# Optimization experiments

Hardware: AMD Instinct MI355X
Metric: run time of the kernel (lower is better)

Reference implementation:

```python
import jax, jax.numpy as jnp
import numpy as np

B, N, C, K3, KNN = 4, 4096, 128, 3, 16
SCALE = 1.0 / np.sqrt(C)  # attention uses sqrt(embed_dim)
EPS = 1e-5


def _knn_idx(x, k):
    # squared euclidean distances (monotone in cdist), topk smallest
    x2 = jnp.sum(x * x, axis=-1)                       # [B,N]
    d2 = x2[:, :, None] + x2[:, None, :] - 2.0 * jnp.einsum('bnd,bmd->bnm', x, x)
    _, idx = jax.lax.top_k(-d2, k)                     # [B,N,k]
    return idx


def _gather(x, idx):
    # knn_gather: x [B,N,D], idx [B,N,k] -> [B,N,k,D]
    return jax.vmap(lambda xb, ib: xb[ib])(x, idx)


def _attn(q_in, kv_in, Wq, Wk, Wv):
    # q_in [B,N,D], kv_in [B,N,k,D]; torch Linear: x @ W.T
    Q = q_in @ Wq.T
    Kt = kv_in @ Wk.T
    V = kv_in @ Wv.T
    scores = jnp.einsum('bnkd,bnd->bnk', Kt, Q) * SCALE
    a = jax.nn.softmax(scores, axis=-1)
    return jnp.einsum('bnk,bnkd->bnd', a, V)


def _ln(x, g, b):
    mu = jnp.mean(x, axis=-1, keepdims=True)
    var = jnp.mean((x - mu) ** 2, axis=-1, keepdims=True)
    return (x - mu) * jax.lax.rsqrt(var + EPS) * g + b


def setup_inputs() -> dict:
    key = jax.random.key(0)
    ks = jax.random.split(key, 20)
    s = 0.05
    inp = {
        'src': jax.random.normal(ks[0], (B, N, K3), dtype=jnp.float32),
        'tgt': jax.random.normal(ks[1], (B, N, C), dtype=jnp.float32),
        'Wq0': jax.random.normal(ks[2], (C, C), dtype=jnp.float32) * s,
        'Wk0': jax.random.normal(ks[3], (C, C), dtype=jnp.float32) * s,
        'Wv0': jax.random.normal(ks[4], (C, C), dtype=jnp.float32) * s,
        'Wq1': jax.random.normal(ks[5], (C, C), dtype=jnp.float32) * s,
        'Wk1': jax.random.normal(ks[6], (C, C), dtype=jnp.float32) * s,
        'Wv1': jax.random.normal(ks[7], (C, C), dtype=jnp.float32) * s,
        'Wp0': jax.random.normal(ks[8], (C, K3), dtype=jnp.float32) * s,
        'bp0': jnp.zeros((C,), dtype=jnp.float32),
        'Wp1': jax.random.normal(ks[9], (C, C), dtype=jnp.float32) * s,
        'bp1': jnp.zeros((C,), dtype=jnp.float32),
        'Wl': jax.random.normal(ks[10], (C, C), dtype=jnp.float32) * s,
        'bl': jnp.zeros((C,), dtype=jnp.float32),
        'g0': jnp.ones((C,), dtype=jnp.float32),
        'b0': jnp.zeros((C,), dtype=jnp.float32),
        'g1': jnp.ones((C,), dtype=jnp.float32),
        'b1': jnp.zeros((C,), dtype=jnp.float32),
    }
    return inp


def reference(src, tgt, Wq0, Wk0, Wv0, Wq1, Wk1, Wv1, Wp0, bp0, Wp1, bp1, Wl, bl, g0, b0, g1, b1):
    k = min(KNN, src.shape[1])
    # stage 1: knn on coordinates
    idx = _knn_idx(src, k)
    gather_src = _gather(src, idx)                         # [B,N,k,3]
    residual_src = (src[:, :, None, :] - gather_src) @ Wp0.T + bp0
    gather_tgt = _gather(tgt, idx)                         # [B,N,k,C]
    out = _attn(tgt, residual_src + gather_tgt, Wq0, Wk0, Wv0)
    # stage 2: knn in feature space
    idx2 = _knn_idx(out, k)
    gather_out = _gather(out, idx2)
    residual_out = (out[:, :, None, :] - gather_out) @ Wp1.T + bp1
    out = _attn(out, residual_out + gather_out, Wq1, Wk1, Wv1)
    out_0 = tgt + out
    out_1 = _ln(out_0, g0, b0) @ Wl.T + bl
    out_2 = _ln(tgt + out_1, g1, b1)
    return jnp.transpose(out_2, (1, 0, 2))                 # [N,B,C]
```

## Files before the change

### kernel.cpp

```cpp
#include <hip/hip_runtime.h>
#include <math.h>

#define NB 4
#define NN 4096
#define NC 128
#define NROWS (NB*NN)
#define SCALE_F 0.08838834764831845f

using bf16x8 = __attribute__((ext_vector_type(8))) short;
using f32x4  = __attribute__((ext_vector_type(4))) float;

__device__ __forceinline__ float rl_f(float x, int l) {
    return __int_as_float(__builtin_amdgcn_readlane(__float_as_int(x), l));
}
__device__ __forceinline__ ushort f2bf(float x) {
    unsigned u = __float_as_uint(x);
    return (ushort)((u + 0x7FFF + ((u >> 16) & 1)) >> 16);
}
__device__ __forceinline__ float bf2f(ushort b) { return __uint_as_float(((unsigned)b) << 16); }

__device__ __forceinline__ unsigned long long mkkey(float d2, int idx) {
    unsigned u = __float_as_uint(d2);
    u ^= ((unsigned)((int)u >> 31)) | 0x80000000u;
    return ((unsigned long long)u << 32) | (unsigned)idx;
}

#define DECL16V \
    float v0=INFINITY,v1=INFINITY,v2=INFINITY,v3=INFINITY,v4=INFINITY,v5=INFINITY,v6=INFINITY,v7=INFINITY, \
          v8=INFINITY,v9=INFINITY,v10=INFINITY,v11=INFINITY,v12=INFINITY,v13=INFINITY,v14=INFINITY,v15=INFINITY;

#define INSERT16V(dv) do { float d_=(dv); \
    bool m0=d_<v0,m1=d_<v1,m2=d_<v2,m3=d_<v3,m4=d_<v4,m5=d_<v5,m6=d_<v6,m7=d_<v7, \
         m8=d_<v8,m9=d_<v9,m10=d_<v10,m11=d_<v11,m12=d_<v12,m13=d_<v13,m14=d_<v14,m15=d_<v15; \
    v15=m14?v14:(m15?d_:v15); v14=m13?v13:(m14?d_:v14); v13=m12?v12:(m13?d_:v13); v12=m11?v11:(m12?d_:v12); \
    v11=m10?v10:(m11?d_:v11); v10=m9?v9:(m10?d_:v10); v9 =m8?v8:(m9?d_:v9);  v8 =m7?v7:(m8?d_:v8); \
    v7 =m6?v6:(m7?d_:v7);   v6 =m5?v5:(m6?d_:v6);   v5 =m4?v4:(m5?d_:v5);  v4 =m3?v3:(m4?d_:v4); \
    v3 =m2?v2:(m3?d_:v3);   v2 =m1?v1:(m2?d_:v2);   v1 =m0?v0:(m1?d_:v1);  v0 =m0?d_:v0; } while(0)

#define POP16V(p) do { bool p_=(p); \
    v0=p_?v1:v0; v1=p_?v2:v1; v2=p_?v3:v2; v3=p_?v4:v3; v4=p_?v5:v4; v5=p_?v6:v5; v6=p_?v7:v6; v7=p_?v8:v7; \
    v8=p_?v9:v8; v9=p_?v10:v9; v10=p_?v11:v10; v11=p_?v12:v11; v12=p_?v13:v12; v13=p_?v14:v13; v14=p_?v15:v14; \
    v15=p_?INFINITY:v15; } while(0)

#define KMAX16 0xFFFFFFFFFFFFFFFFull
#define DECL16K \
    unsigned long long K0=KMAX16,K1=KMAX16,K2=KMAX16,K3=KMAX16,K4=KMAX16,K5=KMAX16,K6=KMAX16,K7=KMAX16, \
                       K8=KMAX16,K9=KMAX16,K10=KMAX16,K11=KMAX16,K12=KMAX16,K13=KMAX16,K14=KMAX16,K15=KMAX16;

#define INSERT16K(kv) do { unsigned long long k_=(kv); \
    bool m0=k_<K0,m1=k_<K1,m2=k_<K2,m3=k_<K3,m4=k_<K4,m5=k_<K5,m6=k_<K6,m7=k_<K7, \
         m8=k_<K8,m9=k_<K9,m10=k_<K10,m11=k_<K11,m12=k_<K12,m13=k_<K13,m14=k_<K14,m15=k_<K15; \
    K15=m14?K14:(m15?k_:K15); K14=m13?K13:(m14?k_:K14); K13=m12?K12:(m13?k_:K13); K12=m11?K11:(m12?k_:K12); \
    K11=m10?K10:(m11?k_:K11); K10=m9?K9:(m10?k_:K10);   K9 =m8?K8:(m9?k_:K9);    K8 =m7?K7:(m8?k_:K8); \
    K7 =m6?K6:(m7?k_:K7);     K6 =m5?K5:(m6?k_:K6);     K5 =m4?K4:(m5?k_:K5);    K4 =m3?K3:(m4?k_:K4); \
    K3 =m2?K2:(m3?k_:K3);     K2 =m1?K1:(m2?k_:K2);     K1 =m0?K0:(m1?k_:K1);    K0 =m0?k_:K0; } while(0)

#define POP16K(p) do { bool p_=(p); \
    K0=p_?K1:K0; K1=p_?K2:K1; K2=p_?K3:K2; K3=p_?K4:K3; K4=p_?K5:K4; K5=p_?K6:K5; K6=p_?K7:K6; K7=p_?K8:K7; \
    K8=p_?K9:K8; K9=p_?K10:K9; K10=p_?K11:K10; K11=p_?K12:K11; K12=p_?K13:K12; K13=p_?K14:K13; K14=p_?K15:K14; \
    K15=p_?KMAX16:K15; } while(0)

__global__ void combo_small(const float* __restrict__ Wk0, const float* __restrict__ Wv0,
                            const float* __restrict__ Wp0, const float* __restrict__ bp0,
                            float* __restrict__ WKP0, float* __restrict__ BK0,
                            float* __restrict__ WVP0, float* __restrict__ BV0)
{
    int task = blockIdx.x * 512 + threadIdx.x;
    if (task >= 1024) return;
    int mat = task >> 9; int rem = task & 511;
    int c = rem >> 2, t = rem & 3;
    const float* W = mat ? Wv0 : Wk0;
    float s = 0.f;
    if (t < 3) {
        for (int d = 0; d < 128; ++d) s = fmaf(W[c*128+d], Wp0[d*3+t], s);
        (mat ? WVP0 : WKP0)[c*3+t] = s;
    } else {
        for (int d = 0; d < 128; ++d) s = fmaf(W[c*128+d], bp0[d], s);
        (mat ? BV0 : BK0)[c] = s;
    }
}

__global__ void combo_big(const float* __restrict__ Wk1, const float* __restrict__ Wv1,
                          const float* __restrict__ Wp1, const float* __restrict__ bp1,
                          float* __restrict__ WKD, float* __restrict__ MV1,
                          float* __restrict__ WVD, float* __restrict__ BV1)
{
    int task = blockIdx.x * 256 + threadIdx.x;
    if (task >= 32896) return;
    if (task < 32768) {
        int mat = task >> 14; int rem = task & 16383;
        int c = rem >> 7, tcol = rem & 127;
        const float* W = mat ? Wv1 : Wk1;
        float s = 0.f;
        for (int d = 0; d < 128; ++d) s = fmaf(W[c*128+d], Wp1[d*128+tcol], s);
        if (mat) { MV1[rem] = s; WVD[rem] = Wv1[rem] - s; }
        else     { WKD[rem] = Wk1[rem] - s; }
    } else {
        int c = task - 32768;
        float s = 0.f;
        for (int d = 0; d < 128; ++d) s = fmaf(Wv1[c*128+d], bp1[d], s);
        BV1[c] = s;
    }
}

__global__ void srcproj(const float* __restrict__ src, const float* __restrict__ WKP0,
                        const float* __restrict__ WVP0,
                        float* __restrict__ srcKp, float* __restrict__ srcVp)
{
    int gid = blockIdx.x * 256 + threadIdx.x;
    int i = gid >> 7, c = gid & 127;
    float s0 = src[i*3+0], s1 = src[i*3+1], s2 = src[i*3+2];
    srcKp[gid] = fmaf(s0, WKP0[c*3+0], fmaf(s1, WKP0[c*3+1], s2*WKP0[c*3+2]));
    srcVp[gid] = fmaf(s0, WVP0[c*3+0], fmaf(s1, WVP0[c*3+1], s2*WVP0[c*3+2]));
}

__global__ __launch_bounds__(256) void knn1_kernel(const float* __restrict__ src,
                                                   int* __restrict__ idxout)
{
    int lane = threadIdx.x & 63, wave = threadIdx.x >> 6;
    int b7 = blockIdx.x & 7, sub = blockIdx.x >> 3;
    int batch = b7 >> 1;
    int rib = (sub*2 + (b7 & 1))*4 + wave;
    int row = batch*NN + rib;
    const float* sb = src + batch*NN*3;
    float xi0 = sb[rib*3], xi1 = sb[rib*3+1], xi2 = sb[rib*3+2];

    DECL16V
    for (int it = 0; it < 64; ++it) {
        int j = it*64 + lane;
        float dx = xi0 - sb[j*3], dy = xi1 - sb[j*3+1], dz = xi2 - sb[j*3+2];
        float d2 = fmaf(dx, dx, fmaf(dy, dy, dz*dz));
        if (d2 < v15) INSERT16V(d2);
    }
    float T = INFINITY;
    for (int t = 0; t < 16; ++t) {
        float g = v0;
#pragma unroll
        for (int off = 1; off < 64; off <<= 1) g = fminf(g, __shfl_xor(g, off, 64));
        unsigned long long b = __ballot(v0 == g);
        int f = __ffsll((long long)b) - 1;
        POP16V(lane == f);
        T = g;
    }
    unsigned long long below_mask = (lane == 63) ? 0x7fffffffffffffffull : ((1ull << lane) - 1ull);
    int base = 0;
    for (int it = 0; it < 64; ++it) {
        int j = it*64 + lane;
        float dx = xi0 - sb[j*3], dy = xi1 - sb[j*3+1], dz = xi2 - sb[j*3+2];
        float d2 = fmaf(dx, dx, fmaf(dy, dy, dz*dz));
        unsigned long long blt = __ballot(d2 < T);
        if (d2 < T) idxout[row*16 + base + __popcll(blt & below_mask)] = j;
        base += __popcll(blt);
    }
    for (int it = 0; it < 64 && base < 16; ++it) {
        int j = it*64 + lane;
        float dx = xi0 - sb[j*3], dy = xi1 - sb[j*3+1], dz = xi2 - sb[j*3+2];
        float d2 = fmaf(dx, dx, fmaf(dy, dy, dz*dz));
        unsigned long long beq = __ballot(d2 == T);
        int bel = __popcll(beq & below_mask);
        if (d2 == T && base + bel < 16) idxout[row*16 + base + bel] = j;
        base += __popcll(beq);
    }
}

__device__ __forceinline__ void matmul128_body(const float* __restrict__ X,
                                               const float* __restrict__ W,
                                               const float* __restrict__ S,
                                               float* __restrict__ Y)
{
    __shared__ float WL[128*128];
    int tid = threadIdx.x;
    for (int f = tid; f < 16384; f += 256) {
        int c = f >> 7, d = f & 127;
        WL[d*128 + (c ^ (d & 14))] = W[f];
    }
    __syncthreads();
    int lane = tid & 63, wave = tid >> 6;
#pragma unroll
    for (int it = 0; it < 2; ++it) {
        int row0 = blockIdx.x*32 + it*16 + wave*4;
        float2 xp[4];
#pragma unroll
        for (int r = 0; r < 4; ++r) {
            xp[r] = *(const float2*)&X[(row0+r)*128 + 2*lane];
        }
        float2 acc[4];
#pragma unroll
        for (int r = 0; r < 4; ++r) { acc[r].x = 0.f; acc[r].y = 0.f; }
#pragma unroll 8
        for (int dh = 0; dh < 64; ++dh) {
            int cidx = (2*lane) ^ ((2*dh) & 14);
            float2 wa = *(const float2*)&WL[(2*dh)*128 + cidx];
            float2 wb = *(const float2*)&WL[(2*dh+1)*128 + cidx];
#pragma unroll
            for (int r = 0; r < 4; ++r) {
                float xa = rl_f(xp[r].x, dh);
                float xb = rl_f(xp[r].y, dh);
                acc[r].x = fmaf(xa, wa.x, acc[r].x);
                acc[r].y = fmaf(xa, wa.y, acc[r].y);
                acc[r].x = fmaf(xb, wb.x, acc[r].x);
                acc[r].y = fmaf(xb, wb.y, acc[r].y);
            }
        }
#pragma unroll
        for (int r = 0; r < 4; ++r) {
            float2 o = acc[r];
            if (S != nullptr) {
                float2 s2 = *(const float2*)&S[(row0+r)*128 + 2*lane];
                o.x -= s2.x; o.y -= s2.y;
            }
            *(float2*)&Y[(row0+r)*128 + 2*lane] = o;
        }
    }
}

__global__ __launch_bounds__(256) void matmul128x3s(
    const float* __restrict__ X,
    const float* __restrict__ W0, const float* __restrict__ W1, const float* __restrict__ W2,
    const float* __restrict__ S1, const float* __restrict__ S2,
    float* __restrict__ Y0, float* __restrict__ Y1, float* __restrict__ Y2)
{
    if (blockIdx.y == 0)      matmul128_body(X, W0, nullptr, Y0);
    else if (blockIdx.y == 1) matmul128_body(X, W1, S1, Y1);
    else                      matmul128_body(X, W2, S2, Y2);
}

__global__ __launch_bounds__(256) void matmul128x4(
    const float* __restrict__ X,
    const float* __restrict__ W0, const float* __restrict__ W1,
    const float* __restrict__ W2, const float* __restrict__ W3,
    float* __restrict__ Y0, float* __restrict__ Y1,
    float* __restrict__ Y2, float* __restrict__ Y3)
{
    const float* W; float* Y;
    switch (blockIdx.y) {
        case 0: W = W0; Y = Y0; break;
        case 1: W = W1; Y = Y1; break;
        case 2: W = W2; Y = Y2; break;
        default: W = W3; Y = Y3; break;
    }
    matmul128_body(X, W, nullptr, Y);
}

__global__ __launch_bounds__(512) void attn_kernel(
    const float* __restrict__ Q,  const float* __restrict__ GK, const float* __restrict__ GV,
    const float* __restrict__ BASE, const float* __restrict__ bv,
    const int* __restrict__ idx, float* __restrict__ outp, float* __restrict__ x2out,
    ushort* __restrict__ xh, ushort* __restrict__ xl)
{
    int tid = threadIdx.x;
    int lane = tid & 63, wave = tid >> 6;
    int xcd = blockIdx.x & 7, sub = blockIdx.x >> 3;
    int batch = xcd >> 1;
    int band = sub*2 + (xcd & 1);
    int rgrp = lane >> 4;
    int dimg = lane & 15;
    int rib = band*32 + wave*4 + rgrp;
    int row = batch*NN + rib;
    int d0 = dimg*8;
    int gbase = lane & 48;
    const float* GKb = GK + (size_t)batch*NN*NC;
    const float* GVb = GV + (size_t)batch*NN*NC;

    float4 q0 = *(const float4*)&Q[(size_t)row*NC + d0];
    float4 q1 = *(const float4*)&Q[(size_t)row*NC + d0 + 4];
    int jv = idx[row*16 + dimg];

    float sc[16];
#pragma unroll
    for (int k = 0; k < 16; ++k) {
        int j = __shfl(jv, gbase + k, 64);
        const float* gk = &GKb[(size_t)j*NC + d0];
        float4 g0 = *(const float4*)gk;
        float4 g1 = *(const float4*)(gk + 4);
        float p = fmaf(q0.x, g0.x, fmaf(q0.y, g0.y, fmaf(q0.z, g0.z, fmaf(q0.w, g0.w,
                  fmaf(q1.x, g1.x, fmaf(q1.y, g1.y, fmaf(q1.z, g1.z, q1.w*g1.w)))))));
#pragma unroll
        for (int off = 1; off < 16; off <<= 1) p += __shfl_xor(p, off, 64);
        sc[k] = p * SCALE_F;
    }
    float m = sc[0];
#pragma unroll
    for (int k = 1; k < 16; ++k) m = fmaxf(m, sc[k]);
    float wsum = 0.f, w[16];
#pragma unroll
    for (int k = 0; k < 16; ++k) { w[k] = expf(sc[k] - m); wsum += w[k]; }
    float inv = 1.f / wsum;

    float4 a0 = {0.f,0.f,0.f,0.f}, a1 = {0.f,0.f,0.f,0.f};
#pragma unroll
    for (int k = 0; k < 16; ++k) {
        int j = __shfl(jv, gbase + k, 64);
        const float* gv = &GVb[(size_t)j*NC + d0];
        float4 v0 = *(const float4*)gv;
        float4 v1 = *(const float4*)(gv + 4);
        float a = w[k] * inv;
        a0.x = fmaf(a, v0.x, a0.x); a0.y = fmaf(a, v0.y, a0.y);
        a0.z = fmaf(a, v0.z, a0.z); a0.w = fmaf(a, v0.w, a0.w);
        a1.x = fmaf(a, v1.x, a1.x); a1.y = fmaf(a, v1.y, a1.y);
        a1.z = fmaf(a, v1.z, a1.z); a1.w = fmaf(a, v1.w, a1.w);
    }
    float4 b0 = *(const float4*)&BASE[(size_t)row*NC + d0];
    float4 b1 = *(const float4*)&BASE[(size_t)row*NC + d0 + 4];
    float4 c0 = *(const float4*)&bv[d0];
    float4 c1 = *(const float4*)&bv[d0 + 4];
    a0.x += b0.x + c0.x; a0.y += b0.y + c0.y; a0.z += b0.z + c0.z; a0.w += b0.w + c0.w;
    a1.x += b1.x + c1.x; a1.y += b1.y + c1.y; a1.z += b1.z + c1.z; a1.w += b1.w + c1.w;
    *(float4*)&outp[(size_t)row*NC + d0]     = a0;
    *(float4*)&outp[(size_t)row*NC + d0 + 4] = a1;

    if (x2out != nullptr) {
        float x2 = fmaf(a0.x, a0.x, fmaf(a0.y, a0.y, fmaf(a0.z, a0.z, fmaf(a0.w, a0.w,
                   fmaf(a1.x, a1.x, fmaf(a1.y, a1.y, fmaf(a1.z, a1.z, a1.w*a1.w)))))));
#pragma unroll
        for (int off = 1; off < 16; off <<= 1) x2 += __shfl_xor(x2, off, 64);
        if (dimg == 0) x2out[row] = x2;
    }
    if (xh != nullptr) {
        ushort h0 = f2bf(a0.x), h1 = f2bf(a0.y), h2 = f2bf(a0.z), h3 = f2bf(a0.w);
        ushort h4 = f2bf(a1.x), h5 = f2bf(a1.y), h6 = f2bf(a1.z), h7 = f2bf(a1.w);
        uint4 ph;
        ph.x = (unsigned)h0 | ((unsigned)h1 << 16);
        ph.y = (unsigned)h2 | ((unsigned)h3 << 16);
        ph.z = (unsigned)h4 | ((unsigned)h5 << 16);
        ph.w = (unsigned)h6 | ((unsigned)h7 << 16);
        *(uint4*)&xh[(size_t)row*NC + d0] = ph;
        ushort l0 = f2bf(a0.x - bf2f(h0)), l1 = f2bf(a0.y - bf2f(h1));
        ushort l2 = f2bf(a0.z - bf2f(h2)), l3 = f2bf(a0.w - bf2f(h3));
        ushort l4 = f2bf(a1.x - bf2f(h4)), l5 = f2bf(a1.y - bf2f(h5));
        ushort l6 = f2bf(a1.z - bf2f(h6)), l7 = f2bf(a1.w - bf2f(h7));
        uint4 pl;
        pl.x = (unsigned)l0 | ((unsigned)l1 << 16);
        pl.y = (unsigned)l2 | ((unsigned)l3 << 16);
        pl.z = (unsigned)l4 | ((unsigned)l5 << 16);
        pl.w = (unsigned)l6 | ((unsigned)l7 << 16);
        *(uint4*)&xl[(size_t)row*NC + d0] = pl;
    }
}

#define SCAN_STEP(CP, X2S, REFRESH) do { \
    float4 dd = *(const float4*)&DT[dtrd]; \
    float4 xx = *(const float4*)&(X2S)[slotl*4]; \
    int cb = 0; \
    { float d2 = fmaf(-2.f, dd.x, xx.x); bool p = d2 <= Trow; \
      unsigned long long bal = __ballot(p); unsigned grp = (unsigned)(bal >> grpsh) & 0xFFFFu; \
      if (p) BUF[srow][cb + __popc(grp & lowm)] = mkkey(d2, (CP) + slotl*4 + 0); \
      cb += __popc(grp); } \
    { float d2 = fmaf(-2.f, dd.y, xx.y); bool p = d2 <= Trow; \
      unsigned long long bal = __ballot(p); unsigned grp = (unsigned)(bal >> grpsh) & 0xFFFFu; \
      if (p) BUF[srow][cb + __popc(grp & lowm)] = mkkey(d2, (CP) + slotl*4 + 1); \
      cb += __popc(grp); } \
    { float d2 = fmaf(-2.f, dd.z, xx.z); bool p = d2 <= Trow; \
      unsigned long long bal = __ballot(p); unsigned grp = (unsigned)(bal >> grpsh) & 0xFFFFu; \
      if (p) BUF[srow][cb + __popc(grp & lowm)] = mkkey(d2, (CP) + slotl*4 + 2); \
      cb += __popc(grp); } \
    { float d2 = fmaf(-2.f, dd.w, xx.w); bool p = d2 <= Trow; \
      unsigned long long bal = __ballot(p); unsigned grp = (unsigned)(bal >> grpsh) & 0xFFFFu; \
      if (p) BUF[srow][cb + __popc(grp & lowm)] = mkkey(d2, (CP) + slotl*4 + 3); \
      cb += __popc(grp); } \
    _Pragma("unroll") \
    for (int r = 0; r < 4; ++r) { \
        int ii = r*16 + slotl; \
        if (ii < cb) { \
            unsigned long long k = BUF[srow][ii]; \
            if (k < K15) INSERT16K(k); \
        } \
    } \
    if (REFRESH) { \
        unsigned long long tk = K15; \
        _Pragma("unroll") \
        for (int off = 1; off < 16; off <<= 1) { \
            unsigned long long o = __shfl_xor(tk, off, 64); \
            tk = (o < tk) ? o : tk; \
        } \
        unsigned uu = (unsigned)(tk >> 32); \
        uu = (uu > 0xFF800000u) ? 0xFF800000u : uu; \
        uu = (uu & 0x80000000u) ? (uu ^ 0x80000000u) : ~uu; \
        Trow = __uint_as_float(uu); \
    } \
} while (0)

__global__ __launch_bounds__(512, 2) void knn2_kernel(const ushort* __restrict__ XHg,
                                                      const ushort* __restrict__ XLg,
                                                      const float* __restrict__ x2g,
                                                      int* __restrict__ idxout)
{
    __shared__ __align__(16) ushort XCH[64*128];
    __shared__ __align__(16) ushort XCL[64*128];
    __shared__ __align__(16) float  DT[32*64];
    __shared__ unsigned long long   BUF[32][65];
    __shared__ __align__(16) float  X2T[2][64];
    int tid = threadIdx.x;
    int lane = tid & 63, wave = tid >> 6;
    int xcd = blockIdx.x & 7, sub = blockIdx.x >> 3;
    int batch = xcd >> 1;
    int band = sub*2 + (xcd & 1);
    const ushort* XHb = XHg + (size_t)batch*NN*NC;
    const ushort* XLb = XLg + (size_t)batch*NN*NC;
    const float*  x2b = x2g + (size_t)batch*NN;
    int r0 = band*32;

    int rowblk = wave & 1, colblk = wave >> 1;
    int dbase = (lane >> 4) * 8;
    int gr = r0 + rowblk*16 + (lane & 15);
    bf16x8 AH[4], AL[4];
#pragma unroll
    for (int ks = 0; ks < 4; ++ks) {
        AH[ks] = *(const bf16x8*)&XHb[(size_t)gr*NC + ks*32 + dbase];
        AL[ks] = *(const bf16x8*)&XLb[(size_t)gr*NC + ks*32 + dbase];
    }
    int cB = colblk*16 + (lane & 15);
    int colw = colblk*16 + (lane & 15);

    int srow = tid >> 4, slotl = tid & 15;
    int grpsh = lane & 48;
    unsigned lowm = (1u << slotl) - 1u;
    int dtrd = srow*64 + ((slotl*4 + 4*srow) & 63);
    float Trow = INFINITY;
    DECL16K

    for (int t = 0; t < 64; ++t) {
        int c0 = t*64;
        __syncthreads();
#pragma unroll
        for (int i = 0; i < 2; ++i) {
            int qq = tid + 512*i;
            int c = qq >> 4, d8 = qq & 15;
            int widx = c*128 + ((d8*8) ^ ((c & 7) << 3));
            *(uint4*)&XCH[widx] = *(const uint4*)&XHb[(size_t)(c0 + c)*NC + d8*8];
            *(uint4*)&XCL[widx] = *(const uint4*)&XLb[(size_t)(c0 + c)*NC + d8*8];
        }
        if (tid < 64) X2T[t & 1][tid] = x2b[c0 + tid];
        if (t > 0) {
            const float* x2s = X2T[(t - 1) & 1];
            SCAN_STEP(c0 - 64, x2s, 1);
        }
        __syncthreads();
        f32x4 acc = {0.f, 0.f, 0.f, 0.f};
#pragma unroll
        for (int ks = 0; ks < 4; ++ks) {
            int bidx = cB*128 + ((ks*32 + dbase) ^ ((cB & 7) << 3));
            bf16x8 bh = *(const bf16x8*)&XCH[bidx];
            bf16x8 bl = *(const bf16x8*)&XCL[bidx];
            acc = __builtin_amdgcn_mfma_f32_16x16x32_bf16(AH[ks], bh, acc, 0, 0, 0);
            acc = __builtin_amdgcn_mfma_f32_16x16x32_bf16(AL[ks], bh, acc, 0, 0, 0);
            acc = __builtin_amdgcn_mfma_f32_16x16x32_bf16(AH[ks], bl, acc, 0, 0, 0);
        }
#pragma unroll
        for (int r2 = 0; r2 < 4; ++r2) {
            int rA = rowblk*16 + (lane >> 4)*4 + r2;
            DT[rA*64 + (((colw & ~3) + 4*rA) & 63) + (colw & 3)] = acc[r2];
        }
    }
    __syncthreads();
    {
        const float* x2s = X2T[1];
        SCAN_STEP(63*64, x2s, 0);
    }
    int grow = batch*NN + r0 + srow;
    for (int tt = 0; tt < 16; ++tt) {
        unsigned long long g = K0;
#pragma unroll
        for (int off = 1; off < 16; off <<= 1) {
            unsigned long long o = __shfl_xor(g, off, 64);
            g = (o < g) ? o : g;
        }
        bool win = (K0 == g);
        if (win) idxout[grow*16 + tt] = (int)(unsigned)(g & 0xFFFFFFFFull);
        POP16K(win);
    }
}

__global__ __launch_bounds__(256) void final_kernel(
    const float* __restrict__ tgt, const float* __restrict__ att,
    const float* __restrict__ Wl, const float* __restrict__ bl,
    const float* __restrict__ g0, const float* __restrict__ b0,
    const float* __restrict__ g1, const float* __restrict__ b1,
    float* __restrict__ outp)
{
    __shared__ float WL[128*128];
    int tid = threadIdx.x;
    for (int f = tid; f < 16384; f += 256) {
        int c = f >> 7, d = f & 127;
        WL[d*128 + (c ^ (d & 14))] = Wl[f];
    }
    __syncthreads();
    int lane = tid & 63, wave = tid >> 6;
    float2 gg0 = *(const float2*)&g0[2*lane];
    float2 bb0 = *(const float2*)&b0[2*lane];
    float2 gg1 = *(const float2*)&g1[2*lane];
    float2 bb1 = *(const float2*)&b1[2*lane];
    float2 bl2 = *(const float2*)&bl[2*lane];
    for (int it = 0; it < 4; ++it) {
        int row0 = blockIdx.x*64 + it*16 + wave*4;
        float2 tg[4];
        float lnx[4], lny[4];
#pragma unroll
        for (int r = 0; r < 4; ++r) {
            int row = row0 + r;
            tg[r] = *(const float2*)&tgt[row*128 + 2*lane];
            float2 at = *(const float2*)&att[row*128 + 2*lane];
            float ox = tg[r].x + at.x, oy = tg[r].y + at.y;
            float s = ox + oy;
#pragma unroll
            for (int off = 1; off < 64; off <<= 1) s += __shfl_xor(s, off, 64);
            float mu = s * (1.f/128.f);
            float dx = ox - mu, dy = oy - mu;
            float vv = fmaf(dx, dx, dy*dy);
#pragma unroll
            for (int off = 1; off < 64; off <<= 1) vv += __shfl_xor(vv, off, 64);
            float rstd = rsqrtf(vv * (1.f/128.f) + 1e-5f);
            lnx[r] = dx * rstd * gg0.x + bb0.x;
            lny[r] = dy * rstd * gg0.y + bb0.y;
        }
        float2 acc[4];
#pragma unroll
        for (int r = 0; r < 4; ++r) { acc[r].x = 0.f; acc[r].y = 0.f; }
#pragma unroll 8
        for (int dh = 0; dh < 64; ++dh) {
            int cidx = (2*lane) ^ ((2*dh) & 14);
            float2 wa = *(const float2*)&WL[(2*dh)*128 + cidx];
            float2 wb = *(const float2*)&WL[(2*dh+1)*128 + cidx];
#pragma unroll
            for (int r = 0; r < 4; ++r) {
                float xa = rl_f(lnx[r], dh);
                float xb = rl_f(lny[r], dh);
                acc[r].x = fmaf(xa, wa.x, acc[r].x);
                acc[r].y = fmaf(xa, wa.y, acc[r].y);
                acc[r].x = fmaf(xb, wb.x, acc[r].x);
                acc[r].y = fmaf(xb, wb.y, acc[r].y);
            }
        }
#pragma unroll
        for (int r = 0; r < 4; ++r) {
            int row = row0 + r;
            float zx = tg[r].x + acc[r].x + bl2.x;
            float zy = tg[r].y + acc[r].y + bl2.y;
            float s = zx + zy;
#pragma unroll
            for (int off = 1; off < 64; off <<= 1) s += __shfl_xor(s, off, 64);
            float mu = s * (1.f/128.f);
            float dx = zx - mu, dy = zy - mu;
            float vv = fmaf(dx, dx, dy*dy);
#pragma unroll
            for (int off = 1; off < 64; off <<= 1) vv += __shfl_xor(vv, off, 64);
            float rstd = rsqrtf(vv * (1.f/128.f) + 1e-5f);
            float2 res;
            res.x = dx * rstd * gg1.x + bb1.x;
            res.y = dy * rstd * gg1.y + bb1.y;
            int b = row >> 12, n = row & 4095;
            *(float2*)&outp[((size_t)n*NB + b)*128 + 2*lane] = res;
        }
    }
}

extern "C" void kernel_launch(void* const* d_in, const int* in_sizes, int n_in,
                              void* d_out, int out_size, void* d_ws, size_t ws_size,
                              hipStream_t stream)
{
    (void)in_sizes; (void)n_in; (void)out_size; (void)ws_size;
    const float* src = (const float*)d_in[0];
    const float* tgt = (const float*)d_in[1];
    const float* Wq0 = (const float*)d_in[2];
    const float* Wk0 = (const float*)d_in[3];
    const float* Wv0 = (const float*)d_in[4];
    const float* Wq1 = (const float*)d_in[5];
    const float* Wk1 = (const float*)d_in[6];
    const float* Wv1 = (const float*)d_in[7];
    const float* Wp0 = (const float*)d_in[8];
    const float* bp0 = (const float*)d_in[9];
    const float* Wp1 = (const float*)d_in[10];
    const float* bp1 = (const float*)d_in[11];
    const float* Wl  = (const float*)d_in[12];
    const float* bl  = (const float*)d_in[13];
    const float* g0  = (const float*)d_in[14];
    const float* b0  = (const float*)d_in[15];
    const float* g1  = (const float*)d_in[16];
    const float* b1  = (const float*)d_in[17];
    float* out = (float*)d_out;

    float* A0   = (float*)d_ws;
    float* A1   = A0 + 2097152;
    float* A2   = A1 + 2097152;
    float* A3   = A2 + 2097152;
    float* A4   = A3 + 2097152;
    float* OUT1 = A4 + 2097152;
    int*   IDX1 = (int*)(OUT1 + 2097152);
    int*   IDX2 = IDX1 + NROWS*16;
    float* X2G  = (float*)(IDX2 + NROWS*16);
    float* WKP0 = X2G + NROWS;
    float* BK0  = WKP0 + 384;
    float* WVP0 = BK0 + 128;
    float* BV0  = WVP0 + 384;
    float* WKD  = BV0 + 128;
    float* MV1  = WKD + 16384;
    float* WVD  = MV1 + 16384;
    float* BV1  = WVD + 16384;
    ushort* XH  = (ushort*)(BV1 + 128);
    ushort* XL  = XH + (size_t)NROWS*NC;

    combo_small<<<dim3(2), dim3(512), 0, stream>>>(Wk0, Wv0, Wp0, bp0, WKP0, BK0, WVP0, BV0);
    combo_big<<<dim3(129), dim3(256), 0, stream>>>(Wk1, Wv1, Wp1, bp1, WKD, MV1, WVD, BV1);
    srcproj<<<dim3(8192), dim3(256), 0, stream>>>(src, WKP0, WVP0, A3, A4);
    knn1_kernel<<<dim3(4096), dim3(256), 0, stream>>>(src, IDX1);
    matmul128x3s<<<dim3(512, 3), dim3(256), 0, stream>>>(tgt, Wq0, Wk0, Wv0, A3, A4, A0, A1, A2);
    attn_kernel<<<dim3(512), dim3(512), 0, stream>>>(A0, A1, A2, A4, BV0, IDX1, OUT1, X2G, XH, XL);
    knn2_kernel<<<dim3(512), dim3(512), 0, stream>>>(XH, XL, X2G, IDX2);
    matmul128x4<<<dim3(512, 4), dim3(256), 0, stream>>>(OUT1, Wq1, WKD, WVD, MV1, A0, A1, A2, A3);
    attn_kernel<<<dim3(512), dim3(512), 0, stream>>>(A0, A1, A2, A3, BV1, IDX2, OUT1, nullptr, nullptr, nullptr);
    final_kernel<<<dim3(256), dim3(256), 0, stream>>>(tgt, OUT1, Wl, bl, g0, b0, g1, b1, out);
}
```

Measured before the change: 499.9 us.

## Replace FP32 scalar projection GEMMs with split-bf16 MFMA GEMM

Replaces the scalar FP32 readlane-based 128x128 projection matmuls with an MFMA kernel that splits inputs and weights into bf16 high and low parts and sums three products, approximating FP32 accuracy. It adds kernels that pre-split the weights and the tgt input. The second-stage GEMM reuses the XH/XL split already emitted by the first attention kernel. This moves the projection work from FP32 vector ALUs to matrix cores, at the cost of extra conversion launches and a small precision loss from dropping the low-times-low term.

```diff
diff --git a/kernel.cpp b/kernel.cpp
--- a/kernel.cpp
+++ b/kernel.cpp
@@ -103,6 +103,46 @@
     }
 }
 
+__global__ void split7(const float* __restrict__ W0, const float* __restrict__ W1,
+                       const float* __restrict__ W2, const float* __restrict__ W3,
+                       const float* __restrict__ W4, const float* __restrict__ W5,
+                       const float* __restrict__ W6,
+                       ushort* __restrict__ WSH, ushort* __restrict__ WSL)
+{
+    int y = blockIdx.y;
+    const float* W;
+    switch (y) {
+        case 0: W = W0; break; case 1: W = W1; break; case 2: W = W2; break;
+        case 3: W = W3; break; case 4: W = W4; break; case 5: W = W5; break;
+        default: W = W6; break;
+    }
+    int i = blockIdx.x*256 + threadIdx.x;
+    float v = W[i];
+    ushort h = f2bf(v);
+    WSH[y*16384 + i] = h;
+    WSL[y*16384 + i] = f2bf(v - bf2f(h));
+}
+
+__global__ void splitx(const float* __restrict__ X, ushort* __restrict__ XH,
+                       ushort* __restrict__ XL)
+{
+    int i = (blockIdx.x*256 + threadIdx.x) * 8;
+    float4 a = *(const float4*)&X[i];
+    float4 b = *(const float4*)&X[i+4];
+    ushort h0=f2bf(a.x),h1=f2bf(a.y),h2=f2bf(a.z),h3=f2bf(a.w);
+    ushort h4=f2bf(b.x),h5=f2bf(b.y),h6=f2bf(b.z),h7=f2bf(b.w);
+    uint4 ph;
+    ph.x=(unsigned)h0|((unsigned)h1<<16); ph.y=(unsigned)h2|((unsigned)h3<<16);
+    ph.z=(unsigned)h4|((unsigned)h5<<16); ph.w=(unsigned)h6|((unsigned)h7<<16);
+    *(uint4*)&XH[i] = ph;
+    ushort l0=f2bf(a.x-bf2f(h0)),l1=f2bf(a.y-bf2f(h1)),l2=f2bf(a.z-bf2f(h2)),l3=f2bf(a.w-bf2f(h3));
+    ushort l4=f2bf(b.x-bf2f(h4)),l5=f2bf(b.y-bf2f(h5)),l6=f2bf(b.z-bf2f(h6)),l7=f2bf(b.w-bf2f(h7));
+    uint4 pl;
+    pl.x=(unsigned)l0|((unsigned)l1<<16); pl.y=(unsigned)l2|((unsigned)l3<<16);
+    pl.z=(unsigned)l4|((unsigned)l5<<16); pl.w=(unsigned)l6|((unsigned)l7<<16);
+    *(uint4*)&XL[i] = pl;
+}
+
 __global__ void srcproj(const float* __restrict__ src, const float* __restrict__ WKP0,
                         const float* __restrict__ WVP0,
                         float* __restrict__ srcKp, float* __restrict__ srcVp)
@@ -163,83 +203,59 @@
     }
 }
 
-__device__ __forceinline__ void matmul128_body(const float* __restrict__ X,
-                                               const float* __restrict__ W,
-                                               const float* __restrict__ S,
-                                               float* __restrict__ Y)
-{
-    __shared__ float WL[128*128];
-    int tid = threadIdx.x;
-    for (int f = tid; f < 16384; f += 256) {
-        int c = f >> 7, d = f & 127;
-        WL[d*128 + (c ^ (d & 14))] = W[f];
+__global__ __launch_bounds__(256, 2) void gemm128(
+    const ushort* __restrict__ XHg, const ushort* __restrict__ XLg,
+    const ushort* __restrict__ WHb, const ushort* __restrict__ WLb,
+    const float* __restrict__ S1, const float* __restrict__ S2,
+    float* __restrict__ Ybase)
+{
+    __shared__ __align__(16) ushort WHs[128*128];
+    __shared__ __align__(16) ushort WLs[128*128];
+    int tid = threadIdx.x, lane = tid & 63, wave = tid >> 6;
+    int y = blockIdx.y;
+    const ushort* WH = WHb + y*16384;
+    const ushort* WL = WLb + y*16384;
+    float* Y = Ybase + (size_t)y*2097152;
+    const float* S = (y == 1) ? S1 : ((y == 2) ? S2 : nullptr);
+#pragma unroll
+    for (int i = 0; i < 8; ++i) {
+        int q = tid + 256*i;
+        int c = q >> 4, d8 = q & 15;
+        int widx = c*128 + ((d8*8) ^ ((c & 7) << 3));
+        *(uint4*)&WHs[widx] = *(const uint4*)&WH[c*128 + d8*8];
+        *(uint4*)&WLs[widx] = *(const uint4*)&WL[c*128 + d8*8];
+    }
+    int r = blockIdx.x*64 + wave*16 + (lane & 15);
+    int dbase = (lane >> 4) * 8;
+    bf16x8 AH[4], AL[4];
+#pragma unroll
+    for (int ks = 0; ks < 4; ++ks) {
+        AH[ks] = *(const bf16x8*)&XHg[(size_t)r*128 + ks*32 + dbase];
+        AL[ks] = *(const bf16x8*)&XLg[(size_t)r*128 + ks*32 + dbase];
     }
     __syncthreads();
-    int lane = tid & 63, wave = tid >> 6;
-#pragma unroll
-    for (int it = 0; it < 2; ++it) {
-        int row0 = blockIdx.x*32 + it*16 + wave*4;
-        float2 xp[4];
-#pragma unroll
-        for (int r = 0; r < 4; ++r) {
-            xp[r] = *(const float2*)&X[(row0+r)*128 + 2*lane];
-        }
-        float2 acc[4];
-#pragma unroll
-        for (int r = 0; r < 4; ++r) { acc[r].x = 0.f; acc[r].y = 0.f; }
-#pragma unroll 8
-        for (int dh = 0; dh < 64; ++dh) {
-            int cidx = (2*lane) ^ ((2*dh) & 14);
-            float2 wa = *(const float2*)&WL[(2*dh)*128 + cidx];
-            float2 wb = *(const float2*)&WL[(2*dh+1)*128 + cidx];
-#pragma unroll
-            for (int r = 0; r < 4; ++r) {
-                float xa = rl_f(xp[r].x, dh);
-                float xb = rl_f(xp[r].y, dh);
-                acc[r].x = fmaf(xa, wa.x, acc[r].x);
-                acc[r].y = fmaf(xa, wa.y, acc[r].y);
-                acc[r].x = fmaf(xb, wb.x, acc[r].x);
-                acc[r].y = fmaf(xb, wb.y, acc[r].y);
-            }
-        }
-#pragma unroll
-        for (int r = 0; r < 4; ++r) {
-            float2 o = acc[r];
-            if (S != nullptr) {
-                float2 s2 = *(const float2*)&S[(row0+r)*128 + 2*lane];
-                o.x -= s2.x; o.y -= s2.y;
-            }
-            *(float2*)&Y[(row0+r)*128 + 2*lane] = o;
-        }
-    }
-}
-
-__global__ __launch_bounds__(256) void matmul128x3s(
-    const float* __restrict__ X,
-    const float* __restrict__ W0, const float* __restrict__ W1, const float* __restrict__ W2,
-    const float* __restrict__ S1, const float* __restrict__ S2,
-    float* __restrict__ Y0, float* __restrict__ Y1, float* __restrict__ Y2)
-{
-    if (blockIdx.y == 0)      matmul128_body(X, W0, nullptr, Y0);
-    else if (blockIdx.y == 1) matmul128_body(X, W1, S1, Y1);
-    else                      matmul128_body(X, W2, S2, Y2);
-}
-
-__global__ __launch_bounds__(256) void matmul128x4(
-    const float* __restrict__ X,
-    const float* __restrict__ W0, const float* __restrict__ W1,
-    const float* __restrict__ W2, const float* __restrict__ W3,
-    float* __restrict__ Y0, float* __restrict__ Y1,
-    float* __restrict__ Y2, float* __restrict__ Y3)
-{
-    const float* W; float* Y;
-    switch (blockIdx.y) {
-        case 0: W = W0; Y = Y0; break;
-        case 1: W = W1; Y = Y1; break;
-        case 2: W = W2; Y = Y2; break;
-        default: W = W3; Y = Y3; break;
-    }
-    matmul128_body(X, W, nullptr, Y);
+    int rbase = blockIdx.x*64 + wave*16 + (lane >> 4)*4;
+#pragma unroll
+    for (int cb = 0; cb < 8; ++cb) {
+        int cB = cb*16 + (lane & 15);
+        f32x4 acc = {0.f, 0.f, 0.f, 0.f};
+#pragma unroll
+        for (int ks = 0; ks < 4; ++ks) {
+            int bidx = cB*128 + ((ks*32 + dbase) ^ ((cB & 7) << 3));
+            bf16x8 bh = *(const bf16x8*)&WHs[bidx];
+            bf16x8 bl = *(const bf16x8*)&WLs[bidx];
+            acc = __builtin_amdgcn_mfma_f32_16x16x32_bf16(AH[ks], bh, acc, 0, 0, 0);
+            acc = __builtin_amdgcn_mfma_f32_16x16x32_bf16(AL[ks], bh, acc, 0, 0, 0);
+            acc = __builtin_amdgcn_mfma_f32_16x16x32_bf16(AH[ks], bl, acc, 0, 0, 0);
+        }
+#pragma unroll
+        for (int r2 = 0; r2 < 4; ++r2) {
+            int rA = rbase + r2;
+            float o = acc[r2];
+            if (S) o -= S[(size_t)rA*128 + cB];
+            Y[(size_t)rA*128 + cB] = o;
+        }
+    }
 }
 
 __global__ __launch_bounds__(512) void attn_kernel(
@@ -596,17 +612,22 @@
     float* MV1  = WKD + 16384;
     float* WVD  = MV1 + 16384;
     float* BV1  = WVD + 16384;
-    ushort* XH  = (ushort*)(BV1 + 128);
+    ushort* WSH = (ushort*)(BV1 + 128);
+    ushort* WSL = WSH + 7*16384;
+    ushort* XH  = WSL + 7*16384;
     ushort* XL  = XH + (size_t)NROWS*NC;
 
     combo_small<<<dim3(2), dim3(512), 0, stream>>>(Wk0, Wv0, Wp0, bp0, WKP0, BK0, WVP0, BV0);
     combo_big<<<dim3(129), dim3(256), 0, stream>>>(Wk1, Wv1, Wp1, bp1, WKD, MV1, WVD, BV1);
+    split7<<<dim3(64, 7), dim3(256), 0, stream>>>(Wq0, Wk0, Wv0, Wq1, WKD, WVD, MV1, WSH, WSL);
     srcproj<<<dim3(8192), dim3(256), 0, stream>>>(src, WKP0, WVP0, A3, A4);
+    splitx<<<dim3(1024), dim3(256), 0, stream>>>(tgt, XH, XL);
     knn1_kernel<<<dim3(4096), dim3(256), 0, stream>>>(src, IDX1);
-    matmul128x3s<<<dim3(512, 3), dim3(256), 0, stream>>>(tgt, Wq0, Wk0, Wv0, A3, A4, A0, A1, A2);
+    gemm128<<<dim3(256, 3), dim3(256), 0, stream>>>(XH, XL, WSH, WSL, A3, A4, A0);
     attn_kernel<<<dim3(512), dim3(512), 0, stream>>>(A0, A1, A2, A4, BV0, IDX1, OUT1, X2G, XH, XL);
     knn2_kernel<<<dim3(512), dim3(512), 0, stream>>>(XH, XL, X2G, IDX2);
-    matmul128x4<<<dim3(512, 4), dim3(256), 0, stream>>>(OUT1, Wq1, WKD, WVD, MV1, A0, A1, A2, A3);
+    gemm128<<<dim3(256, 4), dim3(256), 0, stream>>>(XH, XL, WSH + 3*16384, WSL + 3*16384,
+                                                    nullptr, nullptr, A0);
     attn_kernel<<<dim3(512), dim3(512), 0, stream>>>(A0, A1, A2, A3, BV1, IDX2, OUT1, nullptr, nullptr, nullptr);
     final_kernel<<<dim3(256), dim3(256), 0, stream>>>(tgt, OUT1, Wl, bl, g0, b0, g1, b1, out);
 }
```

Result: faster. 428.4 us (-14.3%).
